# Kernel optimization log

Measured on AMD Instinct MI355X. Metric: run time of the kernel, lower is better.

## Reference

```python
import jax, jax.numpy as jnp
import numpy as np

B, S, E, H = 2, 2048, 1024, 16
D = E // H

def setup_inputs() -> dict:
    key = jax.random.key(0)
    k1, k2, k3, k4, k5 = jax.random.split(key, 5)
    s = 1.0 / np.sqrt(E)
    return {
        "x": jax.random.normal(k1, (B, S, E), dtype=jnp.float32),
        "wv_w": jax.random.uniform(k2, (E, E), jnp.float32, -s, s),
        "wv_b": jax.random.uniform(k3, (E,), jnp.float32, -s, s),
        "wo_w": jax.random.uniform(k4, (E, E), jnp.float32, -s, s),
        "wo_b": jax.random.uniform(k5, (E,), jnp.float32, -s, s),
    }

def reference(x, wv_w, wv_b, wo_w, wo_b):
    b, s_len, e = x.shape
    # v projection -> (B, H, S, D)
    v = (x @ wv_w.T + wv_b).reshape(b, s_len, H, D).transpose(0, 2, 1, 3)
    # causal mask: True above diagonal (blocked); m = inclusive lower triangle
    causal = jnp.triu(jnp.ones((s_len, s_len), dtype=bool), k=1)
    m = (~causal).astype(x.dtype)
    # per-batch min-max scaling over (h, s, d)
    v_min = v.min(axis=(1, 2, 3), keepdims=True)
    v_max = v.max(axis=(1, 2, 3), keepdims=True)
    v_scaled = (v - v_min) / (v_max - v_min + 1e-8)
    # genetic fitness: masked mean pooling + reciprocal-mean normalization
    summed = jnp.einsum('ij,bhjd->bhid', m, v_scaled)  # (B,H,S,D)
    counts = jnp.maximum(m.sum(axis=1), 1.0)[None, None, :, None]
    phi = summed / counts
    denom = phi + 0.5
    sum_inv = (1.0 / denom).sum(axis=-1, keepdims=True)
    gene_fitness = 1.0 / (denom * sum_inv)  # weight, (B,H,S,D)
    # organism fitness scores
    org = jnp.einsum('bhjd,bhid->bhij', v_scaled, gene_fitness)
    org = jnp.where(causal[None, None], -jnp.inf, org)
    attn = jax.nn.softmax(org, axis=-1)
    out = jnp.einsum('bhij,bhjd->bhid', attn, v)
    out = out.transpose(0, 2, 1, 3).reshape(b, s_len, e)
    return out @ wo_w.T + wo_b
```

## Files before the change

kernel.cpp:

```cpp
#include <hip/hip_runtime.h>
#include <hip/hip_bf16.h>

#define B_ 2
#define S_ 2048
#define E_ 1024
#define H_ 16
#define D_ 64
#define M_ 4096

typedef __bf16 bf16_t;
typedef bf16_t bf16x8 __attribute__((ext_vector_type(8)));
typedef float f32x4 __attribute__((ext_vector_type(4)));
typedef unsigned int u32;

__device__ __forceinline__ f32x4 mfma16(bf16x8 a, bf16x8 b, f32x4 c) {
    return __builtin_amdgcn_mfma_f32_16x16x32_bf16(a, b, c, 0, 0, 0);
}
__device__ __forceinline__ unsigned short f2bf(float f) {
    unsigned int u = __float_as_uint(f);
    unsigned int r = (u + 0x7fffu + ((u >> 16) & 1u)) >> 16;
    return (unsigned short)r;
}
__device__ __forceinline__ float bf2f(unsigned short s) {
    return __uint_as_float(((unsigned int)s) << 16);
}
__device__ __forceinline__ u32 cvt_pk_bf16(float lo, float hi) {
    u32 r;
    asm("v_cvt_pk_bf16_f32 %0, %1, %2" : "=v"(r) : "v"(lo), "v"(hi));
    return r;
}
__device__ __forceinline__ unsigned int fenc(float x) {
    unsigned int u = __float_as_uint(x);
    return (u & 0x80000000u) ? ~u : (u | 0x80000000u);
}
__device__ __forceinline__ float fdec(unsigned int u) {
    return __uint_as_float((u & 0x80000000u) ? (u ^ 0x80000000u) : ~u);
}
__device__ __forceinline__ void gload16(const void* g, void* l) {
    __builtin_amdgcn_global_load_lds((const __attribute__((address_space(1))) u32*)g,
                                     (__attribute__((address_space(3))) u32*)l, 16, 0, 0);
}

__global__ void k_init(unsigned int* mm) {
    int t = threadIdx.x;
    if (t < 2) { mm[t * 2] = 0xFFFFFFFFu; mm[t * 2 + 1] = 0u; }
}

__global__ __launch_bounds__(256) void k_cast(const float* __restrict__ src,
                                              unsigned short* __restrict__ dst, int n8) {
    int i = blockIdx.x * 256 + threadIdx.x;
    if (i >= n8) return;
    const float4* s4 = (const float4*)src;
    float4 a = s4[2 * i], c = s4[2 * i + 1];
    uint4 o;
    o.x = cvt_pk_bf16(a.x, a.y);
    o.y = cvt_pk_bf16(a.z, a.w);
    o.z = cvt_pk_bf16(c.x, c.y);
    o.w = cvt_pk_bf16(c.z, c.w);
    ((uint4*)dst)[i] = o;
}

template <int MODE>
__global__ __launch_bounds__(256, 2) void k_gemm(const unsigned short* __restrict__ A,
                                                 const unsigned short* __restrict__ Bm,
                                                 const float* __restrict__ bias,
                                                 unsigned short* __restrict__ outb,
                                                 unsigned short* __restrict__ vtb,
                                                 float* __restrict__ outf,
                                                 unsigned int* __restrict__ mm) {
    __shared__ __align__(16) unsigned short Asm[2][8192];
    __shared__ __align__(16) unsigned short Bsm[2][8192];
    const int K = 1024;
    int tid = threadIdx.x, lane = tid & 63, wv = tid >> 6;
    int wm = wv >> 1, wn = wv & 1;
    int m0 = blockIdx.x * 128, n0 = blockIdx.y * 128;
    int lrow = lane & 15, lgrp = lane >> 4, sw = lane & 7;
    int r8 = lane >> 3, ch = lane & 7;
    const unsigned short* Ag = A + (size_t)(m0 + wv * 8 + r8) * K + ((ch ^ r8) << 3);
    const unsigned short* Bg = Bm + (size_t)(n0 + wv * 8 + r8) * K + ((ch ^ r8) << 3);

#define STAGE(buf, kk)                                                                     \
    {                                                                                      \
        _Pragma("unroll") for (int i = 0; i < 4; ++i)                                      \
            gload16(Ag + (size_t)(i * 32) * K + (kk), &Asm[buf][(i * 32 + wv * 8) * 64]);  \
        _Pragma("unroll") for (int i = 0; i < 4; ++i)                                      \
            gload16(Bg + (size_t)(i * 32) * K + (kk), &Bsm[buf][(i * 32 + wv * 8) * 64]);  \
    }
#define COMPUTE(buf)                                                                        \
    {                                                                                       \
        _Pragma("unroll") for (int kh = 0; kh < 2; ++kh) {                                  \
            int cp = (((kh << 2) | lgrp) ^ sw) << 3;                                        \
            bf16x8 af[4], bfr[4];                                                           \
            _Pragma("unroll") for (int mt = 0; mt < 4; ++mt)                                \
                af[mt] = *(const bf16x8*)&Asm[buf][(wm * 64 + mt * 16 + lrow) * 64 + cp];   \
            _Pragma("unroll") for (int nt = 0; nt < 4; ++nt)                                \
                bfr[nt] = *(const bf16x8*)&Bsm[buf][(wn * 64 + nt * 16 + lrow) * 64 + cp];  \
            _Pragma("unroll") for (int mt = 0; mt < 4; ++mt)                                \
                _Pragma("unroll") for (int nt = 0; nt < 4; ++nt)                            \
                    acc[mt][nt] = mfma16(af[mt], bfr[nt], acc[mt][nt]);                     \
        }                                                                                   \
    }

    f32x4 acc[4][4];
#pragma unroll
    for (int i = 0; i < 4; ++i)
#pragma unroll
        for (int j = 0; j < 4; ++j) acc[i][j] = (f32x4){0.f, 0.f, 0.f, 0.f};

    STAGE(0, 0);
    STAGE(1, 64);
    for (int t = 0; t < 15; ++t) {
        asm volatile("s_waitcnt vmcnt(8)" ::: "memory");
        __builtin_amdgcn_s_barrier();
        __builtin_amdgcn_sched_barrier(0);
        COMPUTE(t & 1);
        asm volatile("s_waitcnt lgkmcnt(0)" ::: "memory");
        __builtin_amdgcn_s_barrier();
        __builtin_amdgcn_sched_barrier(0);
        if (t < 14) STAGE(t & 1, (t + 2) * 64);
    }
    asm volatile("s_waitcnt vmcnt(0)" ::: "memory");
    __builtin_amdgcn_s_barrier();
    __builtin_amdgcn_sched_barrier(0);
    COMPUTE(1);
#undef STAGE
#undef COMPUTE

    float vmin = 1e30f, vmax = -1e30f;
#pragma unroll
    for (int nt = 0; nt < 4; ++nt) {
        int ncol = n0 + wn * 64 + nt * 16 + lrow;
        float bs = bias[ncol];
#pragma unroll
        for (int mt = 0; mt < 4; ++mt) {
            unsigned int lo = 0, hi = 0;
#pragma unroll
            for (int r = 0; r < 4; ++r) {
                int mrow = m0 + wm * 64 + mt * 16 + lgrp * 4 + r;
                float val = acc[mt][nt][r] + bs;
                if constexpr (MODE == 0) {
                    vmin = fminf(vmin, val);
                    vmax = fmaxf(vmax, val);
                    int b = mrow >> 11, s = mrow & 2047, h = ncol >> 6, d = ncol & 63;
                    unsigned short bfv = f2bf(val);
                    outb[(size_t)((b * 16 + h) * 2048 + s) * 64 + d] = bfv;
                    if (r < 2) lo |= ((unsigned int)bfv) << (16 * r);
                    else       hi |= ((unsigned int)bfv) << (16 * (r - 2));
                } else {
                    outf[(size_t)mrow * 1024 + ncol] = val;
                }
            }
            if constexpr (MODE == 0) {
                int mrow0 = m0 + wm * 64 + mt * 16 + lgrp * 4;
                int b = mrow0 >> 11, s0 = mrow0 & 2047;
                int h = ncol >> 6, d = ncol & 63;
                uint2 pk; pk.x = lo; pk.y = hi;
                *(uint2*)&vtb[((size_t)(b * 16 + h) * 64 + d) * 2048 + s0] = pk;
            }
        }
    }
    if constexpr (MODE == 0) {
#pragma unroll
        for (int m = 1; m < 64; m <<= 1) {
            vmin = fminf(vmin, __shfl_xor(vmin, m));
            vmax = fmaxf(vmax, __shfl_xor(vmax, m));
        }
        if (lane == 0) {
            int b = m0 >> 11;
            atomicMin(&mm[b * 2], fenc(vmin));
            atomicMax(&mm[b * 2 + 1], fenc(vmax));
        }
    }
}

__global__ __launch_bounds__(256) void k_scan1(const unsigned short* __restrict__ vb,
                                               float* __restrict__ ps) {
    int g = blockIdx.x * 4 + (threadIdx.x >> 6);
    int d = threadIdx.x & 63;
    int bh = g >> 6, c = g & 63;
    const unsigned short* src = vb + (size_t)bh * S_ * 64 + (size_t)c * 32 * 64 + d;
    float a0 = 0.f, a1 = 0.f, a2 = 0.f, a3 = 0.f;
#pragma unroll
    for (int i = 0; i < 32; i += 4) {
        a0 += bf2f(src[(size_t)i * 64]);
        a1 += bf2f(src[(size_t)(i + 1) * 64]);
        a2 += bf2f(src[(size_t)(i + 2) * 64]);
        a3 += bf2f(src[(size_t)(i + 3) * 64]);
    }
    ps[(size_t)g * 64 + d] = (a0 + a1) + (a2 + a3);
}

__global__ __launch_bounds__(64) void k_scan2(const float* __restrict__ ps,
                                              float* __restrict__ base) {
    int bh = blockIdx.x;
    int d = threadIdx.x;
    const float* p = ps + (size_t)bh * 64 * 64 + d;
    float* bo = base + (size_t)bh * 64 * 64 + d;
    float vals[64];
#pragma unroll
    for (int c = 0; c < 64; ++c) vals[c] = p[(size_t)c * 64];
    float run = 0.f;
#pragma unroll
    for (int c = 0; c < 64; ++c) {
        float t = vals[c];
        vals[c] = run;
        run += t;
    }
#pragma unroll
    for (int c = 0; c < 64; ++c) bo[(size_t)c * 64] = vals[c];
}

__global__ __launch_bounds__(256) void k_scan3(const unsigned short* __restrict__ vb,
                                               const float* __restrict__ base,
                                               unsigned short* __restrict__ gene,
                                               const unsigned int* __restrict__ mm) {
    int g = blockIdx.x * 4 + (threadIdx.x >> 6);
    int d = threadIdx.x & 63;
    int bh = g >> 6, c = g & 63;
    int b = bh >> 4;
    float vmin = fdec(mm[b * 2]), vmax = fdec(mm[b * 2 + 1]);
    float ir = __fdividef(1.0f, vmax - vmin + 1e-8f);
    float irl = ir * 1.4426950408889634f;
    const unsigned short* src = vb + (size_t)bh * S_ * 64 + (size_t)c * 32 * 64 + d;
    unsigned short* dst = gene + (size_t)bh * S_ * 64 + (size_t)c * 32 * 64 + d;
    float acc = base[(size_t)g * 64 + d];
#pragma unroll 4
    for (int i = 0; i < 32; ++i) {
        int s = c * 32 + i;
        acc += bf2f(src[(size_t)i * 64]);
        float phi = __fdividef(acc, (float)(s + 1));
        float inv = __fdividef(1.0f, (phi - vmin) * ir + 0.5f);
        float rs = inv;
#pragma unroll
        for (int m = 1; m < 64; m <<= 1) rs += __shfl_xor(rs, m);
        dst[(size_t)i * 64] = f2bf(__fdividef(inv, rs) * irl);
    }
}

__global__ __launch_bounds__(256, 4) void k_attn(const unsigned short* __restrict__ gene,
                                                 const unsigned short* __restrict__ vb,
                                                 const unsigned short* __restrict__ vt,
                                                 unsigned short* __restrict__ attn_out,
                                                 const unsigned int* __restrict__ mm) {
    __shared__ __align__(16) unsigned short Vsm[2][4096];
    __shared__ __align__(16) unsigned short Tsm[2][4096];
    __shared__ __align__(16) unsigned short plds[4][1024];
    int tid = threadIdx.x, lane = tid & 63, w = tid >> 6;
    int bid = blockIdx.x;
    int qt = 31 - (bid >> 5);
    int bh = ((bid & 7) << 2) | ((bid >> 3) & 3);
    int i0 = qt * 64 + w * 16;
    int lrow = lane & 15, lgrp = lane >> 4;
    int sx = lrow & 7;
    int r8 = lane >> 3, ch = lane & 7;

    int b = bh >> 4;
    float vmin = fdec(mm[b * 2]), vmax = fdec(mm[b * 2 + 1]);
    float ir = __fdividef(1.0f, vmax - vmin + 1e-8f);
    float C2 = (vmin * ir + 1.0f) * 1.4426950408889634f;

    const unsigned short* gbase = gene + (size_t)bh * S_ * 64;
    const unsigned short* vbase = vb + (size_t)bh * S_ * 64;
    const unsigned short* tbase = vt + (size_t)bh * 64 * S_;

    const unsigned short* Vg = vbase + (size_t)(w * 8 + r8) * 64 + ((ch ^ r8) << 3);
    const unsigned short* Tg = tbase + (size_t)(w * 8 + r8) * S_ + ((ch ^ r8) << 3);

#define ASTAGE(buf, jt_)                                                                  \
    {                                                                                     \
        int j0s = (jt_) << 6;                                                             \
        _Pragma("unroll") for (int i = 0; i < 2; ++i)                                     \
            gload16(Vg + (size_t)(j0s + i * 32) * 64, &Vsm[buf][(i * 32 + w * 8) * 64]);  \
        _Pragma("unroll") for (int i = 0; i < 2; ++i)                                     \
            gload16(Tg + (size_t)(i * 32) * S_ + j0s, &Tsm[buf][(i * 32 + w * 8) * 64]);  \
    }

    bf16x8 ga0 = *(const bf16x8*)(gbase + (size_t)(i0 + lrow) * 64 + lgrp * 8);
    bf16x8 ga1 = *(const bf16x8*)(gbase + (size_t)(i0 + lrow) * 64 + 32 + lgrp * 8);

    f32x4 acc[4];
#pragma unroll
    for (int dn = 0; dn < 4; ++dn) acc[dn] = (f32x4){0.f, 0.f, 0.f, 0.f};
    float lsum = 0.f;

    int njt = qt + 1;
    ASTAGE(0, 0);
    for (int jt = 0; jt < njt; ++jt) {
        int cur = jt & 1;
        asm volatile("s_waitcnt vmcnt(0)" ::: "memory");
        __builtin_amdgcn_s_barrier();
        __builtin_amdgcn_sched_barrier(0);
        if (jt + 1 < njt) ASTAGE(cur ^ 1, jt + 1);
        int j0 = jt << 6;
        __builtin_amdgcn_s_setprio(1);
        f32x4 Sv[4];
#pragma unroll
        for (int n = 0; n < 4; ++n) {
            const unsigned short* vr = &Vsm[cur][(n * 16 + lrow) * 64];
            bf16x8 a0 = *(const bf16x8*)(vr + ((lgrp ^ sx) << 3));
            bf16x8 a1 = *(const bf16x8*)(vr + (((lgrp + 4) ^ sx) << 3));
            f32x4 c = (f32x4){0.f, 0.f, 0.f, 0.f};
            c = mfma16(a0, ga0, c);
            c = mfma16(a1, ga1, c);
            Sv[n] = c;
        }
        bool tail = (jt == njt - 1);
#pragma unroll
        for (int n = 0; n < 4; ++n) {
            float q0 = exp2f(Sv[n][0] - C2);
            float q1 = exp2f(Sv[n][1] - C2);
            float q2 = exp2f(Sv[n][2] - C2);
            float q3 = exp2f(Sv[n][3] - C2);
            if (tail) {
                int ii = i0 + lrow;
                int jj = j0 + n * 16 + 4 * lgrp;
                q0 = (jj     <= ii) ? q0 : 0.f;
                q1 = (jj + 1 <= ii) ? q1 : 0.f;
                q2 = (jj + 2 <= ii) ? q2 : 0.f;
                q3 = (jj + 3 <= ii) ? q3 : 0.f;
            }
            lsum += (q0 + q1) + (q2 + q3);
            uint2 pk;
            pk.x = cvt_pk_bf16(q0, q1);
            pk.y = cvt_pk_bf16(q2, q3);
            int chunk = 2 * n + (lgrp >> 1);
            *(uint2*)&plds[w][lrow * 64 + ((chunk ^ sx) << 3) + ((lgrp & 1) << 2)] = pk;
        }
#pragma unroll
        for (int chk = 0; chk < 2; ++chk) {
            int pc = ((chk * 4 + lgrp) ^ sx) << 3;
            bf16x8 pa = *(const bf16x8*)&plds[w][lrow * 64 + pc];
#pragma unroll
            for (int dn = 0; dn < 4; ++dn) {
                bf16x8 tf = *(const bf16x8*)&Tsm[cur][(dn * 16 + lrow) * 64 + pc];
                acc[dn] = mfma16(tf, pa, acc[dn]);
            }
        }
        __builtin_amdgcn_s_setprio(0);
    }
#undef ASTAGE
    lsum += __shfl_xor(lsum, 16);
    lsum += __shfl_xor(lsum, 32);
    lsum = __fdividef(1.0f, lsum);
    int bb = bh >> 4, h = bh & 15;
    int ii = i0 + lrow;
#pragma unroll
    for (int dn = 0; dn < 4; ++dn) {
        uint2 pk;
        pk.x = cvt_pk_bf16(acc[dn][0] * lsum, acc[dn][1] * lsum);
        pk.y = cvt_pk_bf16(acc[dn][2] * lsum, acc[dn][3] * lsum);
        int e = h * 64 + dn * 16 + lgrp * 4;
        *(uint2*)&attn_out[(size_t)(bb * S_ + ii) * E_ + e] = pk;
    }
}

extern "C" void kernel_launch(void* const* d_in, const int* in_sizes, int n_in,
                              void* d_out, int out_size, void* d_ws, size_t ws_size,
                              hipStream_t stream) {
    const float* x = (const float*)d_in[0];
    const float* wv_w = (const float*)d_in[1];
    const float* wv_b = (const float*)d_in[2];
    const float* wo_w = (const float*)d_in[3];
    const float* wo_b = (const float*)d_in[4];
    float* out = (float*)d_out;

    char* w = (char*)d_ws;
    unsigned short* x_bf = (unsigned short*)(w);
    unsigned short* wv_bf = (unsigned short*)(w + 8388608);
    unsigned short* wo_bf = (unsigned short*)(w + 10485760);
    unsigned short* v_bf = (unsigned short*)(w + 12582912);
    unsigned short* vt_bf = (unsigned short*)(w + 20971520);
    float* ps = (float*)(w + 29360128);
    float* base = (float*)(w + 29884416);
    unsigned short* gene = (unsigned short*)(w + 46137344);
    unsigned short* a_bf = (unsigned short*)(w + 54525952);
    unsigned int* mm = (unsigned int*)(w + 62914560);
    if (ws_size < 62914576) return;

    k_init<<<1, 64, 0, stream>>>(mm);
    k_cast<<<2048, 256, 0, stream>>>(x, x_bf, 524288);
    k_cast<<<512, 256, 0, stream>>>(wv_w, wv_bf, 131072);
    k_cast<<<512, 256, 0, stream>>>(wo_w, wo_bf, 131072);
    k_gemm<0><<<dim3(32, 8), 256, 0, stream>>>(x_bf, wv_bf, wv_b, v_bf, vt_bf, nullptr, mm);
    k_scan1<<<512, 256, 0, stream>>>(v_bf, ps);
    k_scan2<<<32, 64, 0, stream>>>(ps, base);
    k_scan3<<<512, 256, 0, stream>>>(v_bf, base, gene, mm);
    k_attn<<<1024, 256, 0, stream>>>(gene, v_bf, vt_bf, a_bf, mm);
    k_gemm<1><<<dim3(32, 8), 256, 0, stream>>>(a_bf, wo_bf, wo_b, nullptr, nullptr, out, nullptr);
}
```

Measured before the change: 139.5 us.

## Store GEMM operands in K-tiled panel layout for contiguous tile loads

The cast kernels now write bf16 operands in a [K/64][rows][64] panel layout, and the attention kernel writes its output in the matching per-head panel layout. The GEMM's staging loads then fetch each 128x64 tile from one contiguous 16 KB region instead of 128 rows strided by K. This is meant to improve DRAM and TLB locality of the global-to-LDS loads. It adds index arithmetic to the cast and epilogue stores and makes those writes scattered.

```diff
diff --git a/kernel.cpp b/kernel.cpp
--- a/kernel.cpp
+++ b/kernel.cpp
@@ -46,10 +46,13 @@
     if (t < 2) { mm[t * 2] = 0xFFFFFFFFu; mm[t * 2 + 1] = 0u; }
 }
 
-__global__ __launch_bounds__(256) void k_cast(const float* __restrict__ src,
-                                              unsigned short* __restrict__ dst, int n8) {
+__global__ __launch_bounds__(256) void k_castp(const float* __restrict__ src,
+                                               unsigned short* __restrict__ dst,
+                                               int n8, int rows) {
     int i = blockIdx.x * 256 + threadIdx.x;
     if (i >= n8) return;
+    int m = (i * 8) >> 10, k = (i * 8) & 1023;
+    int kt = k >> 6, ko = k & 63;
     const float4* s4 = (const float4*)src;
     float4 a = s4[2 * i], c = s4[2 * i + 1];
     uint4 o;
@@ -57,7 +60,7 @@
     o.y = cvt_pk_bf16(a.z, a.w);
     o.z = cvt_pk_bf16(c.x, c.y);
     o.w = cvt_pk_bf16(c.z, c.w);
-    ((uint4*)dst)[i] = o;
+    *(uint4*)&dst[((size_t)kt * rows + m) * 64 + ko] = o;
 }
 
 template <int MODE>
@@ -70,21 +73,24 @@
                                                  unsigned int* __restrict__ mm) {
     __shared__ __align__(16) unsigned short Asm[2][8192];
     __shared__ __align__(16) unsigned short Bsm[2][8192];
-    const int K = 1024;
+    const size_t AKT = (size_t)M_ * 64;
+    const size_t BKT = (size_t)1024 * 64;
     int tid = threadIdx.x, lane = tid & 63, wv = tid >> 6;
     int wm = wv >> 1, wn = wv & 1;
     int m0 = blockIdx.x * 128, n0 = blockIdx.y * 128;
     int lrow = lane & 15, lgrp = lane >> 4, sw = lane & 7;
     int r8 = lane >> 3, ch = lane & 7;
-    const unsigned short* Ag = A + (size_t)(m0 + wv * 8 + r8) * K + ((ch ^ r8) << 3);
-    const unsigned short* Bg = Bm + (size_t)(n0 + wv * 8 + r8) * K + ((ch ^ r8) << 3);
-
-#define STAGE(buf, kk)                                                                     \
-    {                                                                                      \
-        _Pragma("unroll") for (int i = 0; i < 4; ++i)                                      \
-            gload16(Ag + (size_t)(i * 32) * K + (kk), &Asm[buf][(i * 32 + wv * 8) * 64]);  \
-        _Pragma("unroll") for (int i = 0; i < 4; ++i)                                      \
-            gload16(Bg + (size_t)(i * 32) * K + (kk), &Bsm[buf][(i * 32 + wv * 8) * 64]);  \
+    const unsigned short* Ag = A + (size_t)(m0 + wv * 8 + r8) * 64 + ((ch ^ r8) << 3);
+    const unsigned short* Bg = Bm + (size_t)(n0 + wv * 8 + r8) * 64 + ((ch ^ r8) << 3);
+
+#define STAGE(buf, tt)                                                                        \
+    {                                                                                         \
+        _Pragma("unroll") for (int i = 0; i < 4; ++i)                                         \
+            gload16(Ag + (size_t)(tt)*AKT + (size_t)(i * 32) * 64,                            \
+                    &Asm[buf][(i * 32 + wv * 8) * 64]);                                       \
+        _Pragma("unroll") for (int i = 0; i < 4; ++i)                                         \
+            gload16(Bg + (size_t)(tt)*BKT + (size_t)(i * 32) * 64,                            \
+                    &Bsm[buf][(i * 32 + wv * 8) * 64]);                                       \
     }
 #define COMPUTE(buf)                                                                        \
     {                                                                                       \
@@ -108,7 +114,7 @@
         for (int j = 0; j < 4; ++j) acc[i][j] = (f32x4){0.f, 0.f, 0.f, 0.f};
 
     STAGE(0, 0);
-    STAGE(1, 64);
+    STAGE(1, 1);
     for (int t = 0; t < 15; ++t) {
         asm volatile("s_waitcnt vmcnt(8)" ::: "memory");
         __builtin_amdgcn_s_barrier();
@@ -117,7 +123,7 @@
         asm volatile("s_waitcnt lgkmcnt(0)" ::: "memory");
         __builtin_amdgcn_s_barrier();
         __builtin_amdgcn_sched_barrier(0);
-        if (t < 14) STAGE(t & 1, (t + 2) * 64);
+        if (t < 14) STAGE(t & 1, t + 2);
     }
     asm volatile("s_waitcnt vmcnt(0)" ::: "memory");
     __builtin_amdgcn_s_barrier();
@@ -349,8 +355,7 @@
         uint2 pk;
         pk.x = cvt_pk_bf16(acc[dn][0] * lsum, acc[dn][1] * lsum);
         pk.y = cvt_pk_bf16(acc[dn][2] * lsum, acc[dn][3] * lsum);
-        int e = h * 64 + dn * 16 + lgrp * 4;
-        *(uint2*)&attn_out[(size_t)(bb * S_ + ii) * E_ + e] = pk;
+        *(uint2*)&attn_out[((size_t)h * M_ + bb * S_ + ii) * 64 + dn * 16 + lgrp * 4] = pk;
     }
 }
 
@@ -378,9 +383,9 @@
     if (ws_size < 62914576) return;
 
     k_init<<<1, 64, 0, stream>>>(mm);
-    k_cast<<<2048, 256, 0, stream>>>(x, x_bf, 524288);
-    k_cast<<<512, 256, 0, stream>>>(wv_w, wv_bf, 131072);
-    k_cast<<<512, 256, 0, stream>>>(wo_w, wo_bf, 131072);
+    k_castp<<<2048, 256, 0, stream>>>(x, x_bf, 524288, 4096);
+    k_castp<<<512, 256, 0, stream>>>(wv_w, wv_bf, 131072, 1024);
+    k_castp<<<512, 256, 0, stream>>>(wo_w, wo_bf, 131072, 1024);
     k_gemm<0><<<dim3(32, 8), 256, 0, stream>>>(x_bf, wv_bf, wv_b, v_bf, vt_bf, nullptr, mm);
     k_scan1<<<512, 256, 0, stream>>>(v_bf, ps);
     k_scan2<<<32, 64, 0, stream>>>(ps, base);
```

After: 138.3 us. No clear change (-0.8%).
